# Kernel optimization log

Measured on AMD Instinct MI355X. Metric: run time of the kernel, lower is better.

## Reference

```python
import jax, jax.numpy as jnp
import numpy as np

N, E, IN_CH, HEADS, OUT_CH = 50000, 800000, 128, 4, 64
HC = HEADS * OUT_CH
NEG_SLOPE = 0.2
LN_EPS = 1e-5


def setup_inputs() -> dict:
    key = jax.random.key(0)
    ks = jax.random.split(key, 6)
    x = jax.random.normal(ks[0], (N, IN_CH), dtype=jnp.float32)
    edge_index = jax.random.randint(ks[1], (2, E), 0, N, dtype=jnp.int64)
    W = jax.random.normal(ks[2], (IN_CH, HC), dtype=jnp.float32) * 0.05
    att_src = jax.random.normal(ks[3], (HEADS, OUT_CH), dtype=jnp.float32) * 0.05
    att_dst = jax.random.normal(ks[4], (HEADS, OUT_CH), dtype=jnp.float32) * 0.05
    bias = jnp.zeros((HC,), dtype=jnp.float32)
    gamma = jnp.ones((HC,), dtype=jnp.float32)
    beta = jnp.zeros((HC,), dtype=jnp.float32)
    return {"x": x, "edge_index": edge_index, "W": W, "att_src": att_src,
            "att_dst": att_dst, "bias": bias, "gamma": gamma, "beta": beta}


def reference(x, edge_index, W, att_src, att_dst, bias, gamma, beta):
    n = x.shape[0]
    # add self loops (PyG GATConv default add_self_loops=True)
    loops = jnp.arange(n, dtype=edge_index.dtype)
    src = jnp.concatenate([edge_index[0], loops])  # [E+N]
    dst = jnp.concatenate([edge_index[1], loops])
    # linear transform -> [N, H, C]
    h = (x @ W).reshape(n, HEADS, OUT_CH)
    # per-node attention halves [N, H]
    a_s = jnp.einsum('nhc,hc->nh', h, att_src)
    a_d = jnp.einsum('nhc,hc->nh', h, att_dst)
    # per-edge logits [E', H]
    e = jax.nn.leaky_relu(a_s[src] + a_d[dst], NEG_SLOPE)
    # segment softmax over incoming edges of each target node
    m = jax.ops.segment_max(e, dst, num_segments=n)
    p = jnp.exp(e - m[dst])
    s = jax.ops.segment_sum(p, dst, num_segments=n)
    alpha = p / (s[dst] + 1e-16)  # [E', H]
    # weighted scatter-add of source features
    msg = h[src] * alpha[:, :, None]  # [E', H, C]
    out = jax.ops.segment_sum(msg, dst, num_segments=n).reshape(n, HC) + bias
    # LayerNorm over H*C then ELU
    mu = out.mean(-1, keepdims=True)
    var = out.var(-1, keepdims=True)
    normed = (out - mu) * jax.lax.rsqrt(var + LN_EPS) * gamma + beta
    return jax.nn.elu(normed)
```

## Files before the change

kernel.cpp:

```cpp
#include <hip/hip_runtime.h>
#include <math.h>

#define NNODES 50000
#define EEDGES 800000
#define INCH   128
#define HEADS  4
#define OUTCH  64
#define HC     256
#define NEG_SLOPE 0.2f
#define LN_EPS 1e-5f
#define CAP    64

typedef unsigned int   u32;
typedef unsigned short u16;
typedef __attribute__((ext_vector_type(8))) short short8;
typedef __attribute__((ext_vector_type(4))) float floatx4;

__device__ __forceinline__ u16 f2bf(float f) {
    u32 u = __float_as_uint(f);
    return (u16)((u + 0x7fffu + ((u >> 16) & 1u)) >> 16);
}
__device__ __forceinline__ float bflo(u32 u) { return __uint_as_float(u << 16); }
__device__ __forceinline__ float bfhi(u32 u) { return __uint_as_float(u & 0xffff0000u); }
__device__ __forceinline__ float lrelu(float e) { return fmaxf(e, NEG_SLOPE * e); }

__global__ __launch_bounds__(256) void k_prep(const int* __restrict__ buf,
                                              const float* __restrict__ Wm,
                                              int* __restrict__ flag,
                                              u16* __restrict__ Wt) {
    if (blockIdx.x == 0 && threadIdx.x < 64) {
        int v = buf[2 * threadIdx.x + 1];
        unsigned long long b = __ballot(v != 0);
        if (threadIdx.x == 0) flag[0] = (b == 0ULL) ? 1 : 0;
    }
    int idx = blockIdx.x * 256 + threadIdx.x;
    int n = idx >> 7;
    int k = idx & 127;
    Wt[n * 128 + k] = f2bf(Wm[(size_t)k * HC + n]);
}

__global__ __launch_bounds__(256) void k_build(const int* __restrict__ buf,
                                               const int* __restrict__ flag,
                                               int* __restrict__ cursor,
                                               int* __restrict__ adj) {
    int t = blockIdx.x * 256 + threadIdx.x;
    int e0 = t * 2;
    if (e0 >= EEDGES) return;
    int s0, s1, d0, d1;
    if (flag[0]) {
        int4 sp = *(const int4*)&buf[2 * e0];
        int4 dp = *(const int4*)&buf[2 * EEDGES + 2 * e0];
        s0 = sp.x; s1 = sp.z; d0 = dp.x; d1 = dp.z;
    } else {
        int2 sp = *(const int2*)&buf[e0];
        int2 dp = *(const int2*)&buf[EEDGES + e0];
        s0 = sp.x; s1 = sp.y; d0 = dp.x; d1 = dp.y;
    }
    int p0 = atomicAdd(&cursor[d0], 1);
    if (p0 < CAP) adj[(size_t)d0 * CAP + p0] = s0;
    int p1 = atomicAdd(&cursor[d1], 1);
    if (p1 < CAP) adj[(size_t)d1 * CAP + p1] = s1;
}

#define GM   64
#define ASPA 136
#define CSP  264

__global__ __launch_bounds__(256) void k_gemm_mfma(
        const float* __restrict__ X, const u16* __restrict__ Wt,
        const float* __restrict__ att_s, const float* __restrict__ att_d,
        u16* __restrict__ Hb, float* __restrict__ a_s, float* __restrict__ a_d) {
    __shared__ __align__(16) u16 S[GM * CSP];
    int tid = threadIdx.x;
    int lane = tid & 63;
    int w = tid >> 6;
    int l15 = lane & 15;
    int quad = lane >> 4;
    int rowBase = blockIdx.x * GM;

    {
        int r = tid >> 2;
        int c0 = (tid & 3) * 32;
        int grow = rowBase + r;
        u16* dstp = &S[r * ASPA + c0];
        if (grow < NNODES) {
            const float* xr = &X[(size_t)grow * INCH + c0];
#pragma unroll
            for (int i = 0; i < 8; i++) {
                float4 v = *(const float4*)(xr + i * 4);
                ushort4 b;
                b.x = f2bf(v.x); b.y = f2bf(v.y); b.z = f2bf(v.z); b.w = f2bf(v.w);
                *(ushort4*)(dstp + i * 4) = b;
            }
        } else {
            ushort4 z = {0, 0, 0, 0};
#pragma unroll
            for (int i = 0; i < 8; i++) *(ushort4*)(dstp + i * 4) = z;
        }
    }
    __syncthreads();

    floatx4 acc[4][4];
#pragma unroll
    for (int mt = 0; mt < 4; mt++)
#pragma unroll
        for (int nt = 0; nt < 4; nt++)
#pragma unroll
            for (int r = 0; r < 4; r++) acc[mt][nt][r] = 0.f;
#pragma unroll
    for (int kk = 0; kk < 4; kk++) {
        int kof = kk * 32 + quad * 8;
        short8 b[4];
#pragma unroll
        for (int nt = 0; nt < 4; nt++)
            b[nt] = *(const short8*)&Wt[(size_t)(w * 64 + nt * 16 + l15) * 128 + kof];
        short8 a[4];
#pragma unroll
        for (int mt = 0; mt < 4; mt++)
            a[mt] = *(short8*)&S[(mt * 16 + l15) * ASPA + kof];
#pragma unroll
        for (int mt = 0; mt < 4; mt++)
#pragma unroll
            for (int nt = 0; nt < 4; nt++)
                acc[mt][nt] = __builtin_amdgcn_mfma_f32_16x16x32_bf16(a[mt], b[nt], acc[mt][nt], 0, 0, 0);
    }

    float asf[4], adf[4];
#pragma unroll
    for (int nt = 0; nt < 4; nt++) {
        asf[nt] = att_s[w * 64 + nt * 16 + l15];
        adf[nt] = att_d[w * 64 + nt * 16 + l15];
    }
#pragma unroll
    for (int mt = 0; mt < 4; mt++) {
#pragma unroll
        for (int r = 0; r < 4; r++) {
            float ps = acc[mt][0][r] * asf[0] + acc[mt][1][r] * asf[1] +
                       acc[mt][2][r] * asf[2] + acc[mt][3][r] * asf[3];
            float pd = acc[mt][0][r] * adf[0] + acc[mt][1][r] * adf[1] +
                       acc[mt][2][r] * adf[2] + acc[mt][3][r] * adf[3];
#pragma unroll
            for (int off = 8; off >= 1; off >>= 1) {
                ps += __shfl_xor(ps, off, 64);
                pd += __shfl_xor(pd, off, 64);
            }
            int g = rowBase + mt * 16 + quad * 4 + r;
            if (l15 == 0 && g < NNODES) {
                a_s[g * 4 + w] = ps;
                a_d[g * 4 + w] = pd;
            }
        }
    }

    __syncthreads();
#pragma unroll
    for (int mt = 0; mt < 4; mt++)
#pragma unroll
        for (int nt = 0; nt < 4; nt++)
#pragma unroll
            for (int r = 0; r < 4; r++)
                S[(mt * 16 + quad * 4 + r) * CSP + w * 64 + nt * 16 + l15] =
                    f2bf(acc[mt][nt][r]);
    __syncthreads();
    {
        int r = tid >> 2;
        int c0 = (tid & 3) * 64;
        int g = rowBase + r;
        if (g < NNODES) {
            const u16* srcp = &S[r * CSP + c0];
            u16* dstp = &Hb[(size_t)g * HC + c0];
#pragma unroll
            for (int i = 0; i < 8; i++)
                *(uint4*)(dstp + i * 8) = *(const uint4*)(srcp + i * 8);
        }
    }
}

__global__ __launch_bounds__(256) void k_aggregate(
        const u16* __restrict__ Hb,
        const float* __restrict__ a_s, const float* __restrict__ a_d,
        const int* __restrict__ cursor, const int* __restrict__ adj,
        const float* __restrict__ bias, const float* __restrict__ gamma,
        const float* __restrict__ beta, float* __restrict__ out) {
    __shared__ int   sidxS[4][64];
    __shared__ float alphaS[4][256];
    int tid = threadIdx.x;
    int lane = tid & 63;
    int w = tid >> 6;
    int n = blockIdx.x * 4 + w;
    if (n >= NNODES) return;
    int cnt = cursor[n]; if (cnt > CAP) cnt = CAP;
    const int* adjn = &adj[(size_t)n * CAP];

    int half = lane >> 5;
    int cgrp = lane & 31;
    int hme = cgrp >> 3;

    int sidx = 0;
    bool act = lane < cnt;
    if (act) sidx = adjn[lane];
    uint4 hs = *(const uint4*)&Hb[(size_t)n * HC + cgrp * 8];
    float4 adn = *(const float4*)&a_d[n * 4];
    float4 asn = *(const float4*)&a_s[n * 4];
    float ad[4] = {adn.x, adn.y, adn.z, adn.w};

    float p0 = 0.f, p1 = 0.f, p2 = 0.f, p3 = 0.f;
    if (act) {
        float4 as4 = *(const float4*)&a_s[sidx * 4];
        p0 = __expf(lrelu(as4.x + ad[0]));
        p1 = __expf(lrelu(as4.y + ad[1]));
        p2 = __expf(lrelu(as4.z + ad[2]));
        p3 = __expf(lrelu(as4.w + ad[3]));
    }
    float s0 = p0, s1 = p1, s2 = p2, s3 = p3;
#pragma unroll
    for (int off = 32; off >= 1; off >>= 1) {
        s0 += __shfl_xor(s0, off, 64);
        s1 += __shfl_xor(s1, off, 64);
        s2 += __shfl_xor(s2, off, 64);
        s3 += __shfl_xor(s3, off, 64);
    }
    float q0 = __expf(lrelu(asn.x + ad[0]));
    float q1 = __expf(lrelu(asn.y + ad[1]));
    float q2 = __expf(lrelu(asn.z + ad[2]));
    float q3 = __expf(lrelu(asn.w + ad[3]));
    s0 += q0; s1 += q1; s2 += q2; s3 += q3;
    float i0 = 1.f / (s0 + 1e-16f), i1 = 1.f / (s1 + 1e-16f);
    float i2 = 1.f / (s2 + 1e-16f), i3 = 1.f / (s3 + 1e-16f);

    sidxS[w][lane] = sidx;
    *(float4*)&alphaS[w][lane * 4] = make_float4(p0 * i0, p1 * i1, p2 * i2, p3 * i3);
    __builtin_amdgcn_wave_barrier();

    float Aself = (hme == 0) ? q0 * i0 : (hme == 1) ? q1 * i1
                : (hme == 2) ? q2 * i2 : q3 * i3;
    Aself *= 0.5f;
    float accv[8];
    accv[0] = Aself * bflo(hs.x); accv[1] = Aself * bfhi(hs.x);
    accv[2] = Aself * bflo(hs.y); accv[3] = Aself * bfhi(hs.y);
    accv[4] = Aself * bflo(hs.z); accv[5] = Aself * bfhi(hs.z);
    accv[6] = Aself * bflo(hs.w); accv[7] = Aself * bfhi(hs.w);

    int np = (cnt + 15) >> 4;
    uint4 hva[8], hvb[8];
    auto LD = [&](int it, uint4* hv) {
#pragma unroll
        for (int q = 0; q < 8; q++) {
            int jj = it * 16 + 2 * q + half;
            int si = sidxS[w][jj];
            hv[q] = *(const uint4*)&Hb[(size_t)si * HC + cgrp * 8];
        }
    };
    auto ACC = [&](int it, uint4* hv) {
#pragma unroll
        for (int q = 0; q < 8; q++) {
            int jj = it * 16 + 2 * q + half;
            float A = alphaS[w][jj * 4 + hme];
            accv[0] += A * bflo(hv[q].x); accv[1] += A * bfhi(hv[q].x);
            accv[2] += A * bflo(hv[q].y); accv[3] += A * bfhi(hv[q].y);
            accv[4] += A * bflo(hv[q].z); accv[5] += A * bfhi(hv[q].z);
            accv[6] += A * bflo(hv[q].w); accv[7] += A * bfhi(hv[q].w);
        }
    };
    if (np > 0) {
        LD(0, hva);
        int it = 0;
        while (true) {
            bool more = (it + 1) < np;
            if (more) LD(it + 1, hvb);
            ACC(it, hva);
            if (!more) break;
            ++it;
            more = (it + 1) < np;
            if (more) LD(it + 1, hva);
            ACC(it, hvb);
            if (!more) break;
            ++it;
        }
    }

#pragma unroll
    for (int k2 = 0; k2 < 8; k2++) accv[k2] += __shfl_xor(accv[k2], 32, 64);

    int cb = cgrp * 8;
    float4 b0 = *(const float4*)&bias[cb];
    float4 b1 = *(const float4*)&bias[cb + 4];
    accv[0] += b0.x; accv[1] += b0.y; accv[2] += b0.z; accv[3] += b0.w;
    accv[4] += b1.x; accv[5] += b1.y; accv[6] += b1.z; accv[7] += b1.w;
    float psum = 0.f, psq = 0.f;
#pragma unroll
    for (int k2 = 0; k2 < 8; k2++) { psum += accv[k2]; psq += accv[k2] * accv[k2]; }
#pragma unroll
    for (int off = 16; off >= 1; off >>= 1) {
        psum += __shfl_xor(psum, off, 64);
        psq  += __shfl_xor(psq,  off, 64);
    }
    float mean = psum * (1.f / HC);
    float var  = psq * (1.f / HC) - mean * mean;
    float rstd = rsqrtf(var + LN_EPS);
    float4 g0 = *(const float4*)&gamma[cb];
    float4 g1 = *(const float4*)&gamma[cb + 4];
    float4 e0 = *(const float4*)&beta[cb];
    float4 e1 = *(const float4*)&beta[cb + 4];
    float gv[8] = {g0.x, g0.y, g0.z, g0.w, g1.x, g1.y, g1.z, g1.w};
    float bv[8] = {e0.x, e0.y, e0.z, e0.w, e1.x, e1.y, e1.z, e1.w};
    float o[8];
#pragma unroll
    for (int k2 = 0; k2 < 8; k2++) {
        float v = (accv[k2] - mean) * rstd * gv[k2] + bv[k2];
        o[k2] = (v > 0.f) ? v : (__expf(v) - 1.0f);
    }
    float4 wv = half ? make_float4(o[4], o[5], o[6], o[7])
                     : make_float4(o[0], o[1], o[2], o[3]);
    *(float4*)&out[(size_t)n * HC + cb + half * 4] = wv;
}

extern "C" void kernel_launch(void* const* d_in, const int* in_sizes, int n_in,
                              void* d_out, int out_size, void* d_ws, size_t ws_size,
                              hipStream_t stream) {
    const float* x     = (const float*)d_in[0];
    const int*   ebuf  = (const int*)d_in[1];
    const float* Wm    = (const float*)d_in[2];
    const float* att_s = (const float*)d_in[3];
    const float* att_d = (const float*)d_in[4];
    const float* bias  = (const float*)d_in[5];
    const float* gamma = (const float*)d_in[6];
    const float* beta  = (const float*)d_in[7];
    float* out = (float*)d_out;

    char* ws = (char*)d_ws;
    size_t off = 0;
    auto alloc = [&](size_t bytes) -> void* {
        void* p = ws + off;
        off += (bytes + 255) & ~(size_t)255;
        return p;
    };
    u16* Hb     = (u16*)alloc((size_t)NNODES * HC * 2);
    float* a_s  = (float*)alloc((size_t)NNODES * HEADS * 4);
    float* a_d  = (float*)alloc((size_t)NNODES * HEADS * 4);
    int* cursor = (int*)alloc((size_t)NNODES * 4);
    int* adj    = (int*)alloc((size_t)NNODES * CAP * 4);
    u16* Wt     = (u16*)alloc((size_t)HC * INCH * 2);
    int* flag   = (int*)alloc(4);

    hipMemsetAsync(cursor, 0, (size_t)NNODES * 4, stream);

    k_prep<<<128, 256, 0, stream>>>(ebuf, Wm, flag, Wt);
    k_build<<<(EEDGES / 2 + 255) / 256, 256, 0, stream>>>(ebuf, flag, cursor, adj);

    k_gemm_mfma<<<(NNODES + GM - 1) / GM, 256, 0, stream>>>(
        x, Wt, att_s, att_d, Hb, a_s, a_d);

    k_aggregate<<<(NNODES + 3) / 4, 256, 0, stream>>>(
        Hb, a_s, a_d, cursor, adj, bias, gamma, beta, out);
}
```

Before: 268.2 us.

## Fuse prep into build kernel and simplify aggregate gather loop with occupancy hint

Merges the weight-transpose/flag kernel into the edge-build kernel, with each block computing the int64-layout flag itself in shared memory. This removes one launch and the global flag read. The aggregate kernel's ping-pong double-buffered gather loop becomes a simple per-16-edge loop that loads indices and alphas first, then issues eight gathers. It also gets a launch_bounds occupancy hint of 8, which trades explicit software prefetch for more waves hiding latency and risks register spills. Every build block now redundantly reads the first 128 ints of the edge buffer.

```diff
diff --git a/kernel.cpp b/kernel.cpp
--- a/kernel.cpp
+++ b/kernel.cpp
@@ -24,30 +24,32 @@
 __device__ __forceinline__ float bfhi(u32 u) { return __uint_as_float(u & 0xffff0000u); }
 __device__ __forceinline__ float lrelu(float e) { return fmaxf(e, NEG_SLOPE * e); }
 
-__global__ __launch_bounds__(256) void k_prep(const int* __restrict__ buf,
-                                              const float* __restrict__ Wm,
-                                              int* __restrict__ flag,
-                                              u16* __restrict__ Wt) {
-    if (blockIdx.x == 0 && threadIdx.x < 64) {
+__global__ __launch_bounds__(256) void k_build(const int* __restrict__ buf,
+                                               const float* __restrict__ Wm,
+                                               u16* __restrict__ Wt,
+                                               int* __restrict__ cursor,
+                                               int* __restrict__ adj) {
+    __shared__ int flagS;
+    if (threadIdx.x < 64) {
         int v = buf[2 * threadIdx.x + 1];
         unsigned long long b = __ballot(v != 0);
-        if (threadIdx.x == 0) flag[0] = (b == 0ULL) ? 1 : 0;
-    }
-    int idx = blockIdx.x * 256 + threadIdx.x;
-    int n = idx >> 7;
-    int k = idx & 127;
-    Wt[n * 128 + k] = f2bf(Wm[(size_t)k * HC + n]);
-}
-
-__global__ __launch_bounds__(256) void k_build(const int* __restrict__ buf,
-                                               const int* __restrict__ flag,
-                                               int* __restrict__ cursor,
-                                               int* __restrict__ adj) {
+        if (threadIdx.x == 0) flagS = (b == 0ULL) ? 1 : 0;
+    }
+    __syncthreads();
+    int flag = flagS;
+
+    if (blockIdx.x < 128) {
+        int idx = blockIdx.x * 256 + threadIdx.x;
+        int n = idx >> 7;
+        int k = idx & 127;
+        Wt[n * 128 + k] = f2bf(Wm[(size_t)k * HC + n]);
+    }
+
     int t = blockIdx.x * 256 + threadIdx.x;
     int e0 = t * 2;
     if (e0 >= EEDGES) return;
     int s0, s1, d0, d1;
-    if (flag[0]) {
+    if (flag) {
         int4 sp = *(const int4*)&buf[2 * e0];
         int4 dp = *(const int4*)&buf[2 * EEDGES + 2 * e0];
         s0 = sp.x; s1 = sp.z; d0 = dp.x; d1 = dp.z;
@@ -176,7 +178,7 @@
     }
 }
 
-__global__ __launch_bounds__(256) void k_aggregate(
+__global__ __launch_bounds__(256, 8) void k_aggregate(
         const u16* __restrict__ Hb,
         const float* __restrict__ a_s, const float* __restrict__ a_d,
         const int* __restrict__ cursor, const int* __restrict__ adj,
@@ -241,41 +243,27 @@
     accv[4] = Aself * bflo(hs.z); accv[5] = Aself * bfhi(hs.z);
     accv[6] = Aself * bflo(hs.w); accv[7] = Aself * bfhi(hs.w);
 
-    int np = (cnt + 15) >> 4;
-    uint4 hva[8], hvb[8];
-    auto LD = [&](int it, uint4* hv) {
+    int cnt_pad = (cnt + 15) & ~15;
+    for (int j = 0; j < cnt_pad; j += 16) {
+        int jj[8];
+        int si[8];
+        float Al[8];
 #pragma unroll
         for (int q = 0; q < 8; q++) {
-            int jj = it * 16 + 2 * q + half;
-            int si = sidxS[w][jj];
-            hv[q] = *(const uint4*)&Hb[(size_t)si * HC + cgrp * 8];
-        }
-    };
-    auto ACC = [&](int it, uint4* hv) {
+            jj[q] = j + 2 * q + half;
+            si[q] = sidxS[w][jj[q]];
+            Al[q] = alphaS[w][jj[q] * 4 + hme];
+        }
+        uint4 hv[8];
+#pragma unroll
+        for (int q = 0; q < 8; q++)
+            hv[q] = *(const uint4*)&Hb[(size_t)si[q] * HC + cgrp * 8];
 #pragma unroll
         for (int q = 0; q < 8; q++) {
-            int jj = it * 16 + 2 * q + half;
-            float A = alphaS[w][jj * 4 + hme];
-            accv[0] += A * bflo(hv[q].x); accv[1] += A * bfhi(hv[q].x);
-            accv[2] += A * bflo(hv[q].y); accv[3] += A * bfhi(hv[q].y);
-            accv[4] += A * bflo(hv[q].z); accv[5] += A * bfhi(hv[q].z);
-            accv[6] += A * bflo(hv[q].w); accv[7] += A * bfhi(hv[q].w);
-        }
-    };
-    if (np > 0) {
-        LD(0, hva);
-        int it = 0;
-        while (true) {
-            bool more = (it + 1) < np;
-            if (more) LD(it + 1, hvb);
-            ACC(it, hva);
-            if (!more) break;
-            ++it;
-            more = (it + 1) < np;
-            if (more) LD(it + 1, hva);
-            ACC(it, hvb);
-            if (!more) break;
-            ++it;
+            accv[0] += Al[q] * bflo(hv[q].x); accv[1] += Al[q] * bfhi(hv[q].x);
+            accv[2] += Al[q] * bflo(hv[q].y); accv[3] += Al[q] * bfhi(hv[q].y);
+            accv[4] += Al[q] * bflo(hv[q].z); accv[5] += Al[q] * bfhi(hv[q].z);
+            accv[6] += Al[q] * bflo(hv[q].w); accv[7] += Al[q] * bfhi(hv[q].w);
         }
     }
 
@@ -341,12 +329,10 @@
     int* cursor = (int*)alloc((size_t)NNODES * 4);
     int* adj    = (int*)alloc((size_t)NNODES * CAP * 4);
     u16* Wt     = (u16*)alloc((size_t)HC * INCH * 2);
-    int* flag   = (int*)alloc(4);
 
     hipMemsetAsync(cursor, 0, (size_t)NNODES * 4, stream);
 
-    k_prep<<<128, 256, 0, stream>>>(ebuf, Wm, flag, Wt);
-    k_build<<<(EEDGES / 2 + 255) / 256, 256, 0, stream>>>(ebuf, flag, cursor, adj);
+    k_build<<<(EEDGES / 2 + 255) / 256, 256, 0, stream>>>(ebuf, Wm, Wt, cursor, adj);
 
     k_gemm_mfma<<<(NNODES + GM - 1) / GM, 256, 0, stream>>>(
         x, Wt, att_s, att_d, Hb, a_s, a_d);
```

Measured after the change: 275.2 us. 1.03x slower.
